# Kernel optimization log

Measured on AMD Instinct MI355X. Metric: run time of the kernel, lower is better.

Reference implementation:

```python
import jax, jax.numpy as jnp
import numpy as np

N, CDIM, FDIM, HDIM, K = 16384, 512, 512, 1024, 5
WEIGHT = 5.0
EPS = 1e-20


def _xavier(key, shape, gain):
    fan_in, fan_out = shape[-2], shape[-1]
    std = gain * np.sqrt(2.0 / (fan_in + fan_out))
    return jax.random.normal(key, shape, jnp.float32) * std


def setup_inputs() -> dict:
    key = jax.random.key(0)
    ks = jax.random.split(key, 12)
    g = np.sqrt(2.0)  # relu gain; last layer linear gain=1
    inp = {
        "c": jax.random.normal(ks[0], (N, CDIM), jnp.float32),
        "x": jax.random.normal(ks[1], (N, 3), jnp.float32),
        "noise": jax.random.normal(ks[2], (K, N, FDIM), jnp.float32),
        "gumbel_u": jax.random.uniform(ks[3], (N, K), jnp.float32),
        # probs MLP: cdim -> 1024 -> 1024 -> K
        "pw0": _xavier(ks[4], (CDIM, HDIM), g), "pb0": jnp.zeros((HDIM,), jnp.float32),
        "pw1": _xavier(ks[5], (HDIM, HDIM), g), "pb1": jnp.zeros((HDIM,), jnp.float32),
        "pw2": _xavier(ks[6], (HDIM, K), 1.0), "pb2": jnp.zeros((K,), jnp.float32),
        # K Gaussian MLPs (stacked): cdim -> 1024 -> 1024 -> 2*fdim
        "gw0": _xavier(ks[7], (K, CDIM, HDIM), g), "gb0": jnp.zeros((K, HDIM), jnp.float32),
        "gw1": _xavier(ks[8], (K, HDIM, HDIM), g), "gb1": jnp.zeros((K, HDIM), jnp.float32),
        "gw2": _xavier(ks[9], (K, HDIM, 2 * FDIM), 1.0), "gb2": jnp.zeros((K, 2 * FDIM), jnp.float32),
    }
    return inp


def reference(c, x, noise, gumbel_u, pw0, pb0, pw1, pb1, pw2, pb2,
              gw0, gb0, gw1, gb1, gw2, gb2):
    # mixture probabilities: ps = softmax(probs(c))
    h = jax.nn.relu(c @ pw0 + pb0)
    h = jax.nn.relu(h @ pw1 + pb1)
    logits = h @ pw2 + pb2                      # (N, K)
    ps = jax.nn.softmax(logits, axis=-1)

    # all K Gaussian experts, vectorized over component axis k
    g = jax.nn.relu(jnp.einsum('nc,kch->knh', c, gw0) + gb0[:, None, :])
    g = jax.nn.relu(jnp.einsum('knh,khj->knj', g, gw1) + gb1[:, None, :])
    o = jnp.einsum('knh,khf->knf', g, gw2) + gb2[:, None, :]   # (K, N, 2*FDIM)
    mean, logvar = o[..., :FDIM], o[..., FDIM:]
    sample = mean + noise * jnp.exp(logvar * 0.5)              # (K, N, FDIM)

    # per-row categorical draw with p = ps (Gumbel-max, on-device)
    gumbel = -jnp.log(-jnp.log(gumbel_u + EPS) + EPS)
    idx = jnp.argmax(jnp.log(jax.lax.stop_gradient(ps) + EPS) + gumbel, axis=-1)

    mask = jax.nn.one_hot(idx, K, dtype=ps.dtype) * WEIGHT
    weights = (ps + mask) / (1.0 + WEIGHT)                     # (N, K)
    out = jnp.einsum('nk,knf->nf', weights, sample)            # (N, FDIM)
    return out
```

## Files before the change

### kernel.cpp

```cpp
#include <hip/hip_runtime.h>
#include <cstdint>
#include <cstddef>

#define N_ROWS 16384
#define CDIM_C 512
#define HDIM_C 1024
#define FDIM_C 512
#define KMIX 5

typedef unsigned short u16;
typedef __attribute__((ext_vector_type(8))) short bf16x8;
typedef __attribute__((ext_vector_type(4))) float f32x4;

__device__ __forceinline__ u16 f2bf(float x) {
  unsigned u = __float_as_uint(x);
  unsigned r = (u + 0x7fffu + ((u >> 16) & 1u)) >> 16;
  return (u16)r;
}
__device__ __forceinline__ float bf2f(u16 h) {
  return __uint_as_float(((unsigned)h) << 16);
}

__device__ __forceinline__ void gload_lds16(const u16* g, u16* l) {
  __builtin_amdgcn_global_load_lds((const __attribute__((address_space(1))) void*)g,
                                   (__attribute__((address_space(3))) void*)l,
                                   16, 0, 0);
}

__global__ void split3_kernel(const float* __restrict__ x, u16* __restrict__ P0,
                              u16* __restrict__ P1, u16* __restrict__ P2, size_t n) {
  for (size_t i = (size_t)blockIdx.x * 256 + threadIdx.x; i < n; i += (size_t)gridDim.x * 256) {
    const float v = x[i];
    const u16 h = f2bf(v); const float hf = bf2f(h);
    const u16 m = f2bf(v - hf); const float mf = bf2f(m);
    P0[i] = h; P1[i] = m; P2[i] = f2bf(v - hf - mf);
  }
}

template <int NP, bool PERM>
__global__ void transp_split_kernel(const float* __restrict__ W, u16* __restrict__ P0,
                                    u16* __restrict__ P1, u16* __restrict__ P2,
                                    int R, int C) {
  __shared__ float t[32][33];
  const int bz = blockIdx.z;
  const float* Wz = W + (size_t)bz * R * C;
  const size_t oofs = (size_t)bz * R * C;
  const int r0 = blockIdx.x * 32, c0 = blockIdx.y * 32;
  const int tx = threadIdx.x, ty = threadIdx.y;
#pragma unroll
  for (int i = 0; i < 4; ++i)
    t[ty + i * 8][tx] = Wz[(size_t)(r0 + ty + i * 8) * C + c0 + tx];
  __syncthreads();
#pragma unroll
  for (int i = 0; i < 4; ++i) {
    const int c_raw = c0 + ty + i * 8, r = r0 + tx;
    const int c = PERM ? ((c_raw < FDIM_C) ? (c_raw * 2) : ((c_raw - FDIM_C) * 2 + 1)) : c_raw;
    const float x = t[tx][ty + i * 8];
    const size_t idx = oofs + (size_t)c * R + r;
    const u16 h = f2bf(x);
    P0[idx] = h;
    const float hf = bf2f(h);
    const u16 m = f2bf(x - hf);
    P1[idx] = m;
    if (NP >= 3) {
      const float mf = bf2f(m);
      P2[idx] = f2bf(x - hf - mf);
    }
  }
}

template <int NA, int NB, int NT, bool RELU, int OSPL, int BPC>
__global__ __launch_bounds__(256, BPC) void gemm_split(
    const u16* __restrict__ A0, const u16* __restrict__ A1, const u16* __restrict__ A2,
    const u16* __restrict__ B0, const u16* __restrict__ B1, const u16* __restrict__ B2,
    const float* __restrict__ bias, float* __restrict__ outF,
    u16* __restrict__ O0, u16* __restrict__ O1, u16* __restrict__ O2,
    int Nc, int Kd) {
  __shared__ u16 lds[(NA + NB) * 4096];
  const int tid = threadIdx.x;
  const int lane = tid & 63;
  const int wave = tid >> 6;
  const int wm = wave >> 1, wn = wave & 1;

  const int nwg = (int)(gridDim.x * gridDim.y);
  const int orig = (int)(blockIdx.y * gridDim.x + blockIdx.x);
  const int cpx = nwg >> 3;
  const int wg = (orig & 7) * cpx + (orig >> 3);
  const int col0 = (wg & 7) * 128;
  const int row0 = (wg >> 3) * 128;

  const u16* Ap[3] = {A0, A1, A2};
  const u16* Bp[3] = {B0, B1, B2};
  constexpr int TA[6] = {0, 0, 1, 1, 0, 2};
  constexpr int TB[6] = {0, 1, 0, 1, 2, 0};

  f32x4 acc[4][4] = {};
  const int kb = lane >> 4;
  const int rl = lane & 15;
  const int nSteps = Kd >> 5;

  for (int kt = 0; kt < nSteps; ++kt) {
    const int k0 = kt << 5;
    __syncthreads();
#pragma unroll
    for (int p = 0; p < NA + NB; ++p) {
      const u16* gp = (p < NA) ? Ap[p] : Bp[p - NA];
      const int rb = (p < NA) ? row0 : col0;
      u16* lbase = &lds[p * 4096];
#pragma unroll
      for (int it = 0; it < 2; ++it) {
        const int sbase = it * 256 + wave * 64;
        const int slot = sbase + lane;
        const int skb = slot >> 7;
        const int sr = slot & 127;
        gload_lds16(gp + (size_t)(rb + sr) * Kd + (k0 + skb * 8), lbase + sbase * 8);
      }
    }
    __syncthreads();

    bf16x8 aF[NA][4];
    bf16x8 bF[NB][4];
#pragma unroll
    for (int p = 0; p < NA; ++p)
#pragma unroll
      for (int i = 0; i < 4; ++i)
        aF[p][i] = *(const bf16x8*)&lds[p * 4096 + (kb * 128 + wm * 64 + i * 16 + rl) * 8];
#pragma unroll
    for (int p = 0; p < NB; ++p)
#pragma unroll
      for (int j = 0; j < 4; ++j)
        bF[p][j] = *(const bf16x8*)&lds[(NA + p) * 4096 + (kb * 128 + wn * 64 + j * 16 + rl) * 8];
#pragma unroll
    for (int t = 0; t < NT; ++t)
#pragma unroll
      for (int i = 0; i < 4; ++i)
#pragma unroll
        for (int j = 0; j < 4; ++j)
          acc[i][j] = __builtin_amdgcn_mfma_f32_16x16x32_bf16(
              aF[TA[t]][i], bF[TB[t]][j], acc[i][j], 0, 0, 0);
  }

#pragma unroll
  for (int i = 0; i < 4; ++i)
#pragma unroll
    for (int j = 0; j < 4; ++j)
#pragma unroll
      for (int r = 0; r < 4; ++r) {
        const int row = row0 + wm * 64 + i * 16 + (lane >> 4) * 4 + r;
        const int col = col0 + wn * 64 + j * 16 + (lane & 15);
        float y = acc[i][j][r] + bias[col];
        if (RELU) y = fmaxf(y, 0.0f);
        const size_t idx = (size_t)row * Nc + col;
        if constexpr (OSPL == 0) {
          outF[idx] = y;
        } else {
          const u16 h = f2bf(y);
          const float hf = bf2f(h);
          const u16 m = f2bf(y - hf);
          O0[idx] = h;
          O1[idx] = m;
          if constexpr (OSPL == 3) {
            const float mf = bf2f(m);
            O2[idx] = f2bf(y - hf - mf);
          }
        }
      }
}

template <bool RELU, int OSPL, int MIX>
__global__ __launch_bounds__(256, 2) void gemm_wide(
    const u16* __restrict__ A0, const u16* __restrict__ A1,
    const u16* __restrict__ B0, const u16* __restrict__ B1,
    const float* __restrict__ bias, float* __restrict__ outF,
    u16* __restrict__ O0, u16* __restrict__ O1,
    const float* __restrict__ noise_k, const float* __restrict__ wvec,
    float* __restrict__ mixout, int kidx, int Kd) {
  __shared__ __align__(16) u16 lds[24576];
  const int tid = threadIdx.x;
  const int lane = tid & 63;
  const int wave = tid >> 6;
  const int wm = wave >> 1, wn = wave & 1;
  const int hi4 = lane >> 4, rl = lane & 15;

  const int nwg = (int)(gridDim.x * gridDim.y);
  const int orig = (int)(blockIdx.y * gridDim.x + blockIdx.x);
  const int cpx = nwg >> 3;
  const int wg = (orig & 7) * cpx + (orig >> 3);
  const int col0 = (wg & 7) * 128;
  const int row0 = (wg >> 3) * 256;

  const u16* Ap[2] = {A0, A1};
  const u16* Bp[2] = {B0, B1};

  f32x4 acc[8][4] = {};
  bf16x8 aR[8], bR[4];
  const int nSteps = Kd >> 5;

  auto ldA = [&](int p) {
#pragma unroll
    for (int i = 0; i < 8; ++i)
      aR[i] = *(const bf16x8*)&lds[p * 8192 + (hi4 * 256 + wm * 128 + i * 16 + rl) * 8];
  };
  auto ldB = [&](int q) {
#pragma unroll
    for (int j = 0; j < 4; ++j)
      bR[j] = *(const bf16x8*)&lds[16384 + q * 4096 + (hi4 * 128 + wn * 64 + j * 16 + rl) * 8];
  };
  auto FMA = [&]() {
#pragma unroll
    for (int i = 0; i < 8; ++i)
#pragma unroll
      for (int j = 0; j < 4; ++j)
        acc[i][j] = __builtin_amdgcn_mfma_f32_16x16x32_bf16(aR[i], bR[j], acc[i][j], 0, 0, 0);
  };

  for (int kt = 0; kt < nSteps; ++kt) {
    const int ko = kt << 5;
    __syncthreads();
#pragma unroll
    for (int p = 0; p < 2; ++p)
#pragma unroll
      for (int it = 0; it < 4; ++it) {
        const int sbase = it * 256 + (wave << 6);
        const int slot = sbase + lane;
        gload_lds16(Ap[p] + (size_t)(row0 + (slot & 255)) * Kd + ko + (slot >> 8) * 8,
                    &lds[p * 8192 + sbase * 8]);
      }
#pragma unroll
    for (int q = 0; q < 2; ++q)
#pragma unroll
      for (int it = 0; it < 2; ++it) {
        const int sbase = it * 256 + (wave << 6);
        const int slot = sbase + lane;
        gload_lds16(Bp[q] + (size_t)(col0 + (slot & 127)) * Kd + ko + (slot >> 7) * 8,
                    &lds[16384 + q * 4096 + sbase * 8]);
      }
    __syncthreads();

    ldA(1); ldB(0); FMA();
    ldA(0);         FMA();
    ldB(1);         FMA();
  }

#pragma unroll
  for (int i = 0; i < 8; ++i)
#pragma unroll
    for (int j = 0; j < 4; ++j)
#pragma unroll
      for (int r = 0; r < 4; ++r) {
        const int row = row0 + wm * 128 + i * 16 + hi4 * 4 + r;
        const int col = col0 + wn * 64 + j * 16 + rl;
        if constexpr (MIX > 0) {
          const int f = col >> 1;
          const int ocol = (col & 1) ? (f + FDIM_C) : f;
          const float y = acc[i][j][r] + bias[ocol];
          const float other = __shfl_xor(y, 1);
          if (!(lane & 1)) {
            const float sample = y + noise_k[(size_t)row * FDIM_C + f] * expf(0.5f * other);
            const float v = wvec[row * KMIX + kidx] * sample;
            float* op = &mixout[(size_t)row * FDIM_C + f];
            if constexpr (MIX == 1) *op = v; else *op += v;
          }
        } else {
          float y = acc[i][j][r] + bias[col];
          if (RELU) y = fmaxf(y, 0.0f);
          const size_t idx = (size_t)row * HDIM_C + col;
          const u16 h = f2bf(y);
          const float hf = bf2f(h);
          O0[idx] = h;
          O1[idx] = f2bf(y - hf);
          (void)outF;
        }
      }
}

__global__ void p2_weights_kernel(const float* __restrict__ h2, const float* __restrict__ pw2,
                                  const float* __restrict__ pb2, const float* __restrict__ gu,
                                  float* __restrict__ w) {
  const int n = blockIdx.x * 4 + (threadIdx.x >> 6);
  const int lane = threadIdx.x & 63;
  const float* hrow = h2 + (size_t)n * HDIM_C;
  double acc[KMIX] = {0, 0, 0, 0, 0};
  const int c0 = lane * 16;
#pragma unroll
  for (int jj = 0; jj < 16; ++jj) {
    const int cc = c0 + jj;
    const double hv = (double)hrow[cc];
#pragma unroll
    for (int kk = 0; kk < KMIX; ++kk)
      acc[kk] += hv * (double)pw2[cc * KMIX + kk];
  }
#pragma unroll
  for (int offs = 32; offs >= 1; offs >>= 1)
#pragma unroll
    for (int kk = 0; kk < KMIX; ++kk)
      acc[kk] += __shfl_down(acc[kk], offs);
  if (lane == 0) {
    double lg[KMIX], mx = -1e300;
#pragma unroll
    for (int kk = 0; kk < KMIX; ++kk) {
      lg[kk] = acc[kk] + (double)pb2[kk];
      if (lg[kk] > mx) mx = lg[kk];
    }
    double e[KMIX], s = 0.0;
#pragma unroll
    for (int kk = 0; kk < KMIX; ++kk) { e[kk] = exp(lg[kk] - mx); s += e[kk]; }
    int idx = 0; double zb = -1e300;
#pragma unroll
    for (int kk = 0; kk < KMIX; ++kk) {
      const double ps = e[kk] / s;
      const double u = (double)gu[n * KMIX + kk];
      const double g = -log(-log(u + 1e-20) + 1e-20);
      const double zz = log(ps + 1e-20) + g;
      if (zz > zb) { zb = zz; idx = kk; }
    }
#pragma unroll
    for (int kk = 0; kk < KMIX; ++kk)
      w[n * KMIX + kk] = (float)((e[kk] / s + (kk == idx ? 5.0 : 0.0)) / 6.0);
  }
}

extern "C" void kernel_launch(void* const* d_in, const int* in_sizes, int n_in,
                              void* d_out, int out_size, void* d_ws, size_t ws_size,
                              hipStream_t stream) {
  const float* c   = (const float*)d_in[0];
  const float* noise = (const float*)d_in[2];
  const float* gu  = (const float*)d_in[3];
  const float* pw0 = (const float*)d_in[4];
  const float* pb0 = (const float*)d_in[5];
  const float* pw1 = (const float*)d_in[6];
  const float* pb1 = (const float*)d_in[7];
  const float* pw2 = (const float*)d_in[8];
  const float* pb2 = (const float*)d_in[9];
  const float* gw0 = (const float*)d_in[10];
  const float* gb0 = (const float*)d_in[11];
  const float* gw1 = (const float*)d_in[12];
  const float* gb1 = (const float*)d_in[13];
  const float* gw2 = (const float*)d_in[14];
  const float* gb2 = (const float*)d_in[15];
  float* out = (float*)d_out;

  char* ws = (char*)d_ws;
  size_t off = 0;
  auto alloc = [&](size_t bytes) -> char* {
    off = (off + 255) & ~(size_t)255;
    char* p = ws + off;
    off += bytes;
    return p;
  };

  const size_t NCp = (size_t)N_ROWS * CDIM_C * 2;
  const size_t NHp = (size_t)N_ROWS * HDIM_C * 2;
  u16* cH = (u16*)alloc(NCp);
  u16* cM = (u16*)alloc(NCp);
  u16* cL = (u16*)alloc(NCp);
  u16* pw0T0 = (u16*)alloc((size_t)CDIM_C * HDIM_C * 2);
  u16* pw0T1 = (u16*)alloc((size_t)CDIM_C * HDIM_C * 2);
  u16* pw0T2 = (u16*)alloc((size_t)CDIM_C * HDIM_C * 2);
  u16* pw1T0 = (u16*)alloc((size_t)HDIM_C * HDIM_C * 2);
  u16* pw1T1 = (u16*)alloc((size_t)HDIM_C * HDIM_C * 2);
  u16* pw1T2 = (u16*)alloc((size_t)HDIM_C * HDIM_C * 2);
  u16* hH = (u16*)alloc(NHp);
  u16* hM = (u16*)alloc(NHp);
  u16* hL = (u16*)alloc(NHp);
  float* h2 = (float*)alloc((size_t)N_ROWS * HDIM_C * 4);
  float* wbuf = (float*)alloc((size_t)N_ROWS * KMIX * 4);
  u16* gw0T0 = (u16*)alloc((size_t)KMIX * CDIM_C * HDIM_C * 2);
  u16* gw0T1 = (u16*)alloc((size_t)KMIX * CDIM_C * HDIM_C * 2);
  u16* gw1T0 = (u16*)alloc((size_t)KMIX * HDIM_C * HDIM_C * 2);
  u16* gw1T1 = (u16*)alloc((size_t)KMIX * HDIM_C * HDIM_C * 2);
  u16* gw2T0 = (u16*)alloc((size_t)KMIX * HDIM_C * HDIM_C * 2);
  u16* gw2T1 = (u16*)alloc((size_t)KMIX * HDIM_C * HDIM_C * 2);
  u16* g2b = (u16*)alloc(NHp);
  u16* g1a = hH;
  u16* g1b = hM;
  u16* g2a = hL;
  (void)ws_size; (void)in_sizes; (void)n_in; (void)out_size;

  split3_kernel<<<2048, 256, 0, stream>>>(c, cH, cM, cL, (size_t)N_ROWS * CDIM_C);
  transp_split_kernel<3, false><<<dim3(CDIM_C / 32, HDIM_C / 32, 1), dim3(32, 8), 0, stream>>>(
      pw0, pw0T0, pw0T1, pw0T2, CDIM_C, HDIM_C);
  transp_split_kernel<3, false><<<dim3(HDIM_C / 32, HDIM_C / 32, 1), dim3(32, 8), 0, stream>>>(
      pw1, pw1T0, pw1T1, pw1T2, HDIM_C, HDIM_C);
  transp_split_kernel<2, false><<<dim3(CDIM_C / 32, HDIM_C / 32, KMIX), dim3(32, 8), 0, stream>>>(
      gw0, gw0T0, gw0T1, nullptr, CDIM_C, HDIM_C);
  transp_split_kernel<2, false><<<dim3(HDIM_C / 32, HDIM_C / 32, KMIX), dim3(32, 8), 0, stream>>>(
      gw1, gw1T0, gw1T1, nullptr, HDIM_C, HDIM_C);
  transp_split_kernel<2, true><<<dim3(HDIM_C / 32, HDIM_C / 32, KMIX), dim3(32, 8), 0, stream>>>(
      gw2, gw2T0, gw2T1, nullptr, HDIM_C, HDIM_C);

  const dim3 ggP(HDIM_C / 128, N_ROWS / 128);
  const dim3 ggG(HDIM_C / 128, N_ROWS / 256);

  gemm_split<3, 3, 6, true, 3, 3><<<ggP, 256, 0, stream>>>(
      cH, cM, cL, pw0T0, pw0T1, pw0T2, pb0, nullptr, hH, hM, hL, HDIM_C, CDIM_C);
  gemm_split<3, 3, 6, true, 0, 3><<<ggP, 256, 0, stream>>>(
      hH, hM, hL, pw1T0, pw1T1, pw1T2, pb1, h2, nullptr, nullptr, nullptr, HDIM_C, HDIM_C);
  p2_weights_kernel<<<N_ROWS / 4, 256, 0, stream>>>(h2, pw2, pb2, gu, wbuf);

  for (int k = 0; k < KMIX; ++k) {
    gemm_wide<true, 2, 0><<<ggG, 256, 0, stream>>>(
        cH, cM,
        gw0T0 + (size_t)k * CDIM_C * HDIM_C, gw0T1 + (size_t)k * CDIM_C * HDIM_C,
        gb0 + k * HDIM_C, nullptr, g1a, g1b,
        nullptr, nullptr, nullptr, 0, CDIM_C);
    gemm_wide<true, 2, 0><<<ggG, 256, 0, stream>>>(
        g1a, g1b,
        gw1T0 + (size_t)k * HDIM_C * HDIM_C, gw1T1 + (size_t)k * HDIM_C * HDIM_C,
        gb1 + k * HDIM_C, nullptr, g2a, g2b,
        nullptr, nullptr, nullptr, 0, HDIM_C);
    if (k == 0)
      gemm_wide<false, 0, 1><<<ggG, 256, 0, stream>>>(
          g2a, g2b,
          gw2T0 + (size_t)k * HDIM_C * HDIM_C, gw2T1 + (size_t)k * HDIM_C * HDIM_C,
          gb2 + k * HDIM_C, nullptr, nullptr, nullptr,
          noise + (size_t)k * N_ROWS * FDIM_C, wbuf, out, k, HDIM_C);
    else
      gemm_wide<false, 0, 2><<<ggG, 256, 0, stream>>>(
          g2a, g2b,
          gw2T0 + (size_t)k * HDIM_C * HDIM_C, gw2T1 + (size_t)k * HDIM_C * HDIM_C,
          gb2 + k * HDIM_C, nullptr, nullptr, nullptr,
          noise + (size_t)k * N_ROWS * FDIM_C, wbuf, out, k, HDIM_C);
  }
}
```

Before: 2.346 ms.

## Widen probs-MLP split-bf16 GEMM to 256-row tiles with B-fragment reuse

Result: slower. 2.593 ms (+10.5%).

```diff
diff --git a/kernel.cpp b/kernel.cpp
--- a/kernel.cpp
+++ b/kernel.cpp
@@ -69,88 +69,90 @@
   }
 }
 
-template <int NA, int NB, int NT, bool RELU, int OSPL, int BPC>
-__global__ __launch_bounds__(256, BPC) void gemm_split(
+template <bool RELU, int OSPL>
+__global__ __launch_bounds__(256, 2) void gemm_pwide(
     const u16* __restrict__ A0, const u16* __restrict__ A1, const u16* __restrict__ A2,
     const u16* __restrict__ B0, const u16* __restrict__ B1, const u16* __restrict__ B2,
     const float* __restrict__ bias, float* __restrict__ outF,
-    u16* __restrict__ O0, u16* __restrict__ O1, u16* __restrict__ O2,
-    int Nc, int Kd) {
-  __shared__ u16 lds[(NA + NB) * 4096];
+    u16* __restrict__ O0, u16* __restrict__ O1, u16* __restrict__ O2, int Kd) {
+  __shared__ __align__(16) u16 lds[36864];
   const int tid = threadIdx.x;
   const int lane = tid & 63;
   const int wave = tid >> 6;
   const int wm = wave >> 1, wn = wave & 1;
+  const int hi4 = lane >> 4, rl = lane & 15;
 
   const int nwg = (int)(gridDim.x * gridDim.y);
   const int orig = (int)(blockIdx.y * gridDim.x + blockIdx.x);
   const int cpx = nwg >> 3;
   const int wg = (orig & 7) * cpx + (orig >> 3);
   const int col0 = (wg & 7) * 128;
-  const int row0 = (wg >> 3) * 128;
+  const int row0 = (wg >> 3) * 256;
 
   const u16* Ap[3] = {A0, A1, A2};
   const u16* Bp[3] = {B0, B1, B2};
-  constexpr int TA[6] = {0, 0, 1, 1, 0, 2};
-  constexpr int TB[6] = {0, 1, 0, 1, 2, 0};
-
-  f32x4 acc[4][4] = {};
-  const int kb = lane >> 4;
-  const int rl = lane & 15;
+
+  f32x4 acc[8][4] = {};
+  bf16x8 bR[4];
   const int nSteps = Kd >> 5;
 
+  const int aoff = (hi4 * 256 + wm * 128 + rl) * 8;
+  const int boff = 24576 + (hi4 * 128 + wn * 64 + rl) * 8;
+
+  auto ldB = [&](int q) {
+#pragma unroll
+    for (int j = 0; j < 4; ++j)
+      bR[j] = *(const bf16x8*)&lds[boff + q * 4096 + j * 128];
+  };
+  auto passA = [&](int p) {
+#pragma unroll
+    for (int i = 0; i < 8; ++i) {
+      const bf16x8 a = *(const bf16x8*)&lds[aoff + p * 8192 + i * 128];
+#pragma unroll
+      for (int j = 0; j < 4; ++j)
+        acc[i][j] = __builtin_amdgcn_mfma_f32_16x16x32_bf16(a, bR[j], acc[i][j], 0, 0, 0);
+    }
+  };
+
   for (int kt = 0; kt < nSteps; ++kt) {
-    const int k0 = kt << 5;
+    const int ko = kt << 5;
     __syncthreads();
 #pragma unroll
-    for (int p = 0; p < NA + NB; ++p) {
-      const u16* gp = (p < NA) ? Ap[p] : Bp[p - NA];
-      const int rb = (p < NA) ? row0 : col0;
-      u16* lbase = &lds[p * 4096];
+    for (int p = 0; p < 3; ++p)
+#pragma unroll
+      for (int it = 0; it < 4; ++it) {
+        const int sbase = it * 256 + (wave << 6);
+        const int slot = sbase + lane;
+        gload_lds16(Ap[p] + (size_t)(row0 + (slot & 255)) * Kd + ko + (slot >> 8) * 8,
+                    &lds[p * 8192 + sbase * 8]);
+      }
+#pragma unroll
+    for (int q = 0; q < 3; ++q)
 #pragma unroll
       for (int it = 0; it < 2; ++it) {
-        const int sbase = it * 256 + wave * 64;
+        const int sbase = it * 256 + (wave << 6);
         const int slot = sbase + lane;
-        const int skb = slot >> 7;
-        const int sr = slot & 127;
-        gload_lds16(gp + (size_t)(rb + sr) * Kd + (k0 + skb * 8), lbase + sbase * 8);
-      }
-    }
+        gload_lds16(Bp[q] + (size_t)(col0 + (slot & 127)) * Kd + ko + (slot >> 7) * 8,
+                    &lds[24576 + q * 4096 + sbase * 8]);
+      }
     __syncthreads();
 
-    bf16x8 aF[NA][4];
-    bf16x8 bF[NB][4];
-#pragma unroll
-    for (int p = 0; p < NA; ++p)
-#pragma unroll
-      for (int i = 0; i < 4; ++i)
-        aF[p][i] = *(const bf16x8*)&lds[p * 4096 + (kb * 128 + wm * 64 + i * 16 + rl) * 8];
-#pragma unroll
-    for (int p = 0; p < NB; ++p)
-#pragma unroll
-      for (int j = 0; j < 4; ++j)
-        bF[p][j] = *(const bf16x8*)&lds[(NA + p) * 4096 + (kb * 128 + wn * 64 + j * 16 + rl) * 8];
-#pragma unroll
-    for (int t = 0; t < NT; ++t)
-#pragma unroll
-      for (int i = 0; i < 4; ++i)
-#pragma unroll
-        for (int j = 0; j < 4; ++j)
-          acc[i][j] = __builtin_amdgcn_mfma_f32_16x16x32_bf16(
-              aF[TA[t]][i], bF[TB[t]][j], acc[i][j], 0, 0, 0);
-  }
-
-#pragma unroll
-  for (int i = 0; i < 4; ++i)
+    ldB(0); passA(0); passA(1); passA(2);
+    ldB(1); passA(0); passA(1);
+    ldB(2); passA(0);
+  }
+
+#pragma unroll
+  for (int i = 0; i < 8; ++i)
 #pragma unroll
     for (int j = 0; j < 4; ++j)
 #pragma unroll
       for (int r = 0; r < 4; ++r) {
-        const int row = row0 + wm * 64 + i * 16 + (lane >> 4) * 4 + r;
-        const int col = col0 + wn * 64 + j * 16 + (lane & 15);
+        const int row = row0 + wm * 128 + i * 16 + hi4 * 4 + r;
+        const int col = col0 + wn * 64 + j * 16 + rl;
         float y = acc[i][j][r] + bias[col];
         if (RELU) y = fmaxf(y, 0.0f);
-        const size_t idx = (size_t)row * Nc + col;
+        const size_t idx = (size_t)row * HDIM_C + col;
         if constexpr (OSPL == 0) {
           outF[idx] = y;
         } else {
@@ -159,10 +161,8 @@
           const u16 m = f2bf(y - hf);
           O0[idx] = h;
           O1[idx] = m;
-          if constexpr (OSPL == 3) {
-            const float mf = bf2f(m);
-            O2[idx] = f2bf(y - hf - mf);
-          }
+          const float mf = bf2f(m);
+          O2[idx] = f2bf(y - hf - mf);
         }
       }
 }
@@ -389,34 +389,33 @@
   transp_split_kernel<2, true><<<dim3(HDIM_C / 32, HDIM_C / 32, KMIX), dim3(32, 8), 0, stream>>>(
       gw2, gw2T0, gw2T1, nullptr, HDIM_C, HDIM_C);
 
-  const dim3 ggP(HDIM_C / 128, N_ROWS / 128);
-  const dim3 ggG(HDIM_C / 128, N_ROWS / 256);
-
-  gemm_split<3, 3, 6, true, 3, 3><<<ggP, 256, 0, stream>>>(
-      cH, cM, cL, pw0T0, pw0T1, pw0T2, pb0, nullptr, hH, hM, hL, HDIM_C, CDIM_C);
-  gemm_split<3, 3, 6, true, 0, 3><<<ggP, 256, 0, stream>>>(
-      hH, hM, hL, pw1T0, pw1T1, pw1T2, pb1, h2, nullptr, nullptr, nullptr, HDIM_C, HDIM_C);
+  const dim3 ggW(HDIM_C / 128, N_ROWS / 256);
+
+  gemm_pwide<true, 3><<<ggW, 256, 0, stream>>>(
+      cH, cM, cL, pw0T0, pw0T1, pw0T2, pb0, nullptr, hH, hM, hL, CDIM_C);
+  gemm_pwide<true, 0><<<ggW, 256, 0, stream>>>(
+      hH, hM, hL, pw1T0, pw1T1, pw1T2, pb1, h2, nullptr, nullptr, nullptr, HDIM_C);
   p2_weights_kernel<<<N_ROWS / 4, 256, 0, stream>>>(h2, pw2, pb2, gu, wbuf);
 
   for (int k = 0; k < KMIX; ++k) {
-    gemm_wide<true, 2, 0><<<ggG, 256, 0, stream>>>(
+    gemm_wide<true, 2, 0><<<ggW, 256, 0, stream>>>(
         cH, cM,
         gw0T0 + (size_t)k * CDIM_C * HDIM_C, gw0T1 + (size_t)k * CDIM_C * HDIM_C,
         gb0 + k * HDIM_C, nullptr, g1a, g1b,
         nullptr, nullptr, nullptr, 0, CDIM_C);
-    gemm_wide<true, 2, 0><<<ggG, 256, 0, stream>>>(
+    gemm_wide<true, 2, 0><<<ggW, 256, 0, stream>>>(
         g1a, g1b,
         gw1T0 + (size_t)k * HDIM_C * HDIM_C, gw1T1 + (size_t)k * HDIM_C * HDIM_C,
         gb1 + k * HDIM_C, nullptr, g2a, g2b,
         nullptr, nullptr, nullptr, 0, HDIM_C);
     if (k == 0)
-      gemm_wide<false, 0, 1><<<ggG, 256, 0, stream>>>(
+      gemm_wide<false, 0, 1><<<ggW, 256, 0, stream>>>(
           g2a, g2b,
           gw2T0 + (size_t)k * HDIM_C * HDIM_C, gw2T1 + (size_t)k * HDIM_C * HDIM_C,
           gb2 + k * HDIM_C, nullptr, nullptr, nullptr,
           noise + (size_t)k * N_ROWS * FDIM_C, wbuf, out, k, HDIM_C);
     else
-      gemm_wide<false, 0, 2><<<ggG, 256, 0, stream>>>(
+      gemm_wide<false, 0, 2><<<ggW, 256, 0, stream>>>(
           g2a, g2b,
           gw2T0 + (size_t)k * HDIM_C * HDIM_C, gw2T1 + (size_t)k * HDIM_C * HDIM_C,
           gb2 + k * HDIM_C, nullptr, nullptr, nullptr,
```
